# Kernel optimization log

Measured on AMD Instinct MI355X. Metric: run time of the kernel, lower is better.

## Reference

```python
import jax, jax.numpy as jnp
import numpy as np

B, T, D, F, E, K = 2, 1024, 1024, 2048, 8, 2

def setup_inputs() -> dict:
    key = jax.random.key(0)
    ks = jax.random.split(key, 9)
    s = 0.02
    return {
        "states": jax.random.normal(ks[0], (B, T, D), dtype=jnp.float32),
        "Wg": jax.random.normal(ks[1], (D, E), dtype=jnp.float32) * s,
        "W_in": jax.random.normal(ks[2], (E, D, F), dtype=jnp.float32) * s,
        "b_in": jnp.zeros((E, F), dtype=jnp.float32),
        "W_scale": jax.random.normal(ks[3], (E, D, F), dtype=jnp.float32) * s,
        "b_scale": jnp.zeros((E, F), dtype=jnp.float32),
        "W_out": jax.random.normal(ks[4], (E, F, D), dtype=jnp.float32) * s,
        "b_out": jnp.zeros((E, D), dtype=jnp.float32),
        "num_selected": K,
    }

def reference(states, Wg, W_in, b_in, W_scale, b_scale, W_out, b_out, num_selected):
    b, t, d = states.shape
    x = states.reshape(-1, d)                      # [N, D]
    n = x.shape[0]
    # router: softmax over experts, then top-k + renormalize
    probs = jax.nn.softmax(x @ Wg, axis=-1)        # [N, E]
    topw, topi = jax.lax.top_k(probs, num_selected)  # [N, K]
    topw = topw / topw.sum(axis=-1, keepdims=True)
    # dense combine weights [N, E]: zero except selected experts
    w_full = jnp.zeros_like(probs).at[jnp.arange(n)[:, None], topi].set(topw)
    # gated-GELU expert MLPs, batched over experts
    h = jnp.einsum('nd,edf->enf', x, W_in) + b_in[:, None, :]       # [E, N, F]
    s = jnp.einsum('nd,edf->enf', x, W_scale) + b_scale[:, None, :]
    inner = jax.nn.gelu(h, approximate=False) * s                    # exact GELU (torch default)
    y = jnp.einsum('enf,efd->end', inner, W_out) + b_out[:, None, :]  # [E, N, D]
    out = jnp.einsum('end,ne->nd', y, w_full)                         # weighted combine
    return out.reshape(b, t, d)
```

## Files before the change

### kernel.cpp

```cpp
#include <hip/hip_runtime.h>
#include <hip/hip_bf16.h>
#include <math.h>

#define N_TOK 2048
#define DIM   1024
#define FF    2048
#define NEXP  8
#define NSLOT (N_TOK * 2)

typedef __attribute__((ext_vector_type(8))) short short8;
typedef __attribute__((ext_vector_type(4))) float f32x4;

__device__ __forceinline__ unsigned short f2bf(float f) {
    unsigned int u = __float_as_uint(f);
    u += 0x7FFFu + ((u >> 16) & 1u);
    return (unsigned short)(u >> 16);
}

__global__ __launch_bounds__(256) void k_router(const float* __restrict__ x,
        const float* __restrict__ Wg, int* __restrict__ hdr,
        int* __restrict__ tok_e, float* __restrict__ tok_w) {
    int wave = threadIdx.x >> 6, lane = threadIdx.x & 63;
    int t = blockIdx.x * 4 + wave;
    float acc[NEXP];
#pragma unroll
    for (int e = 0; e < NEXP; ++e) acc[e] = 0.f;
    const float* xr = x + (size_t)t * DIM;
    for (int d = lane; d < DIM; d += 64) {
        float xv = xr[d];
        const float* wr = Wg + d * NEXP;
#pragma unroll
        for (int e = 0; e < NEXP; ++e) acc[e] += xv * wr[e];
    }
#pragma unroll
    for (int off = 32; off > 0; off >>= 1) {
#pragma unroll
        for (int e = 0; e < NEXP; ++e) acc[e] += __shfl_down(acc[e], off);
    }
    if (lane == 0) {
        int e0 = 0;
#pragma unroll
        for (int e = 1; e < NEXP; ++e) if (acc[e] > acc[e0]) e0 = e;
        int e1 = -1;
#pragma unroll
        for (int e = 0; e < NEXP; ++e) {
            if (e == e0) continue;
            if (e1 < 0 || acc[e] > acc[e1]) e1 = e;
        }
        float w0 = 1.f / (1.f + expf(acc[e1] - acc[e0]));
        tok_e[2 * t] = e0; tok_e[2 * t + 1] = e1;
        tok_w[2 * t] = w0; tok_w[2 * t + 1] = 1.f - w0;
        atomicAdd(&hdr[e0], 1);
        atomicAdd(&hdr[e1], 1);
    }
}

__global__ void k_scan(int* hdr) {
    if (threadIdx.x == 0 && blockIdx.x == 0) {
        int s = 0;
        for (int e = 0; e < NEXP; ++e) {
            hdr[16 + e] = s;
            hdr[8 + e]  = s;
            s += hdr[e];
        }
        hdr[24] = s;
    }
}

__global__ __launch_bounds__(256) void k_assign(const float* __restrict__ x,
        int* __restrict__ hdr, const int* __restrict__ tok_e,
        const float* __restrict__ tok_w, int* __restrict__ tok_slot,
        float* __restrict__ slot_w, unsigned short* __restrict__ xg) {
    __shared__ int sh[2];
    int t = blockIdx.x;
    if (threadIdx.x == 0) {
        int e0 = tok_e[2 * t], e1 = tok_e[2 * t + 1];
        int p0 = atomicAdd(&hdr[8 + e0], 1);
        int p1 = atomicAdd(&hdr[8 + e1], 1);
        tok_slot[2 * t] = p0; tok_slot[2 * t + 1] = p1;
        slot_w[p0] = tok_w[2 * t];
        slot_w[p1] = tok_w[2 * t + 1];
        sh[0] = p0; sh[1] = p1;
    }
    __syncthreads();
    int s0 = sh[0], s1 = sh[1];
    const float4* xr = (const float4*)(x + (size_t)t * DIM);
    float4 v = xr[threadIdx.x];
    ushort4 b;
    b.x = f2bf(v.x); b.y = f2bf(v.y); b.z = f2bf(v.z); b.w = f2bf(v.w);
    ((ushort4*)(xg + (size_t)s0 * DIM))[threadIdx.x] = b;
    ((ushort4*)(xg + (size_t)s1 * DIM))[threadIdx.x] = b;
}

__global__ __launch_bounds__(256) void k_expert_hs(
        const unsigned short* __restrict__ xg,
        const float* __restrict__ Win, const float* __restrict__ Wsc,
        const float* __restrict__ b_in, const float* __restrict__ b_sc,
        const int* __restrict__ hdr, unsigned short* __restrict__ inner) {
    int e = blockIdx.z;
    int cnt = hdr[e];
    int mtile = blockIdx.y;
    if (mtile * 128 >= cnt) return;
    int base = hdr[16 + e];
    int f0 = blockIdx.x * 64;

    __shared__ unsigned short As[128 * 40];
    __shared__ unsigned short Bh[64 * 40];
    __shared__ unsigned short Bs[64 * 40];

    int tid = threadIdx.x;
    int wave = tid >> 6, lane = tid & 63;
    int lr = lane & 15, lq = lane >> 4;
    int wm = (wave >> 1) * 64, wf = (wave & 1) * 32;

    f32x4 acch[4][2], accs[4][2];
#pragma unroll
    for (int mi = 0; mi < 4; ++mi)
#pragma unroll
        for (int fi = 0; fi < 2; ++fi) {
            acch[mi][fi] = (f32x4){0.f, 0.f, 0.f, 0.f};
            accs[mi][fi] = (f32x4){0.f, 0.f, 0.f, 0.f};
        }

    const unsigned short* Arow = xg + (size_t)(base + mtile * 128) * DIM;
    int ar = tid >> 1, ah = (tid & 1) * 16;
    int bf = tid & 63, bkq = tid >> 6;
    const float* WinE = Win + (size_t)e * DIM * FF;
    const float* WscE = Wsc + (size_t)e * DIM * FF;

    for (int k0 = 0; k0 < DIM; k0 += 32) {
        const uint4* asrc = (const uint4*)(Arow + (size_t)ar * DIM + k0 + ah);
        uint4 a0 = asrc[0], a1 = asrc[1];
        const float* ph = WinE + (size_t)(k0 + bkq * 8) * FF + f0 + bf;
        const float* ps = WscE + (size_t)(k0 + bkq * 8) * FF + f0 + bf;
        unsigned int hv[4], sv[4];
#pragma unroll
        for (int j = 0; j < 4; ++j) {
            hv[j] = (unsigned)f2bf(ph[(size_t)(2 * j) * FF]) |
                    ((unsigned)f2bf(ph[(size_t)(2 * j + 1) * FF]) << 16);
            sv[j] = (unsigned)f2bf(ps[(size_t)(2 * j) * FF]) |
                    ((unsigned)f2bf(ps[(size_t)(2 * j + 1) * FF]) << 16);
        }
        __syncthreads();
        *(uint4*)&As[ar * 40 + ah] = a0;
        *(uint4*)&As[ar * 40 + ah + 8] = a1;
        *(uint4*)&Bh[bf * 40 + bkq * 8] = make_uint4(hv[0], hv[1], hv[2], hv[3]);
        *(uint4*)&Bs[bf * 40 + bkq * 8] = make_uint4(sv[0], sv[1], sv[2], sv[3]);
        __syncthreads();

        short8 af[4], bhf[2], bsf[2];
#pragma unroll
        for (int mi = 0; mi < 4; ++mi)
            af[mi] = *(const short8*)&As[(wm + mi * 16 + lr) * 40 + lq * 8];
#pragma unroll
        for (int fi = 0; fi < 2; ++fi) {
            bhf[fi] = *(const short8*)&Bh[(wf + fi * 16 + lr) * 40 + lq * 8];
            bsf[fi] = *(const short8*)&Bs[(wf + fi * 16 + lr) * 40 + lq * 8];
        }
#pragma unroll
        for (int mi = 0; mi < 4; ++mi)
#pragma unroll
            for (int fi = 0; fi < 2; ++fi) {
                acch[mi][fi] = __builtin_amdgcn_mfma_f32_16x16x32_bf16(
                    af[mi], bhf[fi], acch[mi][fi], 0, 0, 0);
                accs[mi][fi] = __builtin_amdgcn_mfma_f32_16x16x32_bf16(
                    af[mi], bsf[fi], accs[mi][fi], 0, 0, 0);
            }
    }

#pragma unroll
    for (int fi = 0; fi < 2; ++fi) {
        int f = f0 + wf + fi * 16 + lr;
        float bi = b_in[e * FF + f];
        float bs2 = b_sc[e * FF + f];
#pragma unroll
        for (int mi = 0; mi < 4; ++mi) {
#pragma unroll
            for (int r = 0; r < 4; ++r) {
                int rl = wm + mi * 16 + lq * 4 + r;
                int grow = mtile * 128 + rl;
                if (grow < cnt) {
                    float h = acch[mi][fi][r] + bi;
                    float s = accs[mi][fi][r] + bs2;
                    float g = 0.5f * h * (1.f + erff(h * 0.70710678f));
                    inner[(size_t)(base + grow) * FF + f] = f2bf(g * s);
                }
            }
        }
    }
}

__global__ __launch_bounds__(256) void k_expert_out(
        const unsigned short* __restrict__ inner,
        const float* __restrict__ Wout, const float* __restrict__ b_out,
        const int* __restrict__ hdr, const float* __restrict__ slot_w,
        float* __restrict__ ybuf) {
    int e = blockIdx.z;
    int cnt = hdr[e];
    int mtile = blockIdx.y;
    if (mtile * 128 >= cnt) return;
    int base = hdr[16 + e];
    int d0 = blockIdx.x * 128;

    __shared__ unsigned short As[128 * 40];
    __shared__ unsigned short Bt[128 * 40];

    int tid = threadIdx.x;
    int wave = tid >> 6, lane = tid & 63;
    int lr = lane & 15, lq = lane >> 4;
    int wm = (wave >> 1) * 64, wn = (wave & 1) * 64;

    f32x4 acc[4][4];
#pragma unroll
    for (int mi = 0; mi < 4; ++mi)
#pragma unroll
        for (int ni = 0; ni < 4; ++ni) acc[mi][ni] = (f32x4){0.f, 0.f, 0.f, 0.f};

    const unsigned short* Arow = inner + (size_t)(base + mtile * 128) * FF;
    int ar = tid >> 1, ah = (tid & 1) * 16;
    int bd = tid & 127, bkq = tid >> 7;
    const float* W = Wout + (size_t)e * FF * DIM;

    for (int k0 = 0; k0 < FF; k0 += 32) {
        const uint4* asrc = (const uint4*)(Arow + (size_t)ar * FF + k0 + ah);
        uint4 a0 = asrc[0], a1 = asrc[1];
        const float* pw = W + (size_t)(k0 + bkq * 16) * DIM + d0 + bd;
        unsigned int wv[8];
#pragma unroll
        for (int j = 0; j < 8; ++j) {
            wv[j] = (unsigned)f2bf(pw[(size_t)(2 * j) * DIM]) |
                    ((unsigned)f2bf(pw[(size_t)(2 * j + 1) * DIM]) << 16);
        }
        __syncthreads();
        *(uint4*)&As[ar * 40 + ah] = a0;
        *(uint4*)&As[ar * 40 + ah + 8] = a1;
        *(uint4*)&Bt[bd * 40 + bkq * 16] = make_uint4(wv[0], wv[1], wv[2], wv[3]);
        *(uint4*)&Bt[bd * 40 + bkq * 16 + 8] = make_uint4(wv[4], wv[5], wv[6], wv[7]);
        __syncthreads();

        short8 af[4], bfm[4];
#pragma unroll
        for (int mi = 0; mi < 4; ++mi)
            af[mi] = *(const short8*)&As[(wm + mi * 16 + lr) * 40 + lq * 8];
#pragma unroll
        for (int ni = 0; ni < 4; ++ni)
            bfm[ni] = *(const short8*)&Bt[(wn + ni * 16 + lr) * 40 + lq * 8];
#pragma unroll
        for (int mi = 0; mi < 4; ++mi)
#pragma unroll
            for (int ni = 0; ni < 4; ++ni)
                acc[mi][ni] = __builtin_amdgcn_mfma_f32_16x16x32_bf16(
                    af[mi], bfm[ni], acc[mi][ni], 0, 0, 0);
    }

#pragma unroll
    for (int ni = 0; ni < 4; ++ni) {
        int d = d0 + wn + ni * 16 + lr;
        float bo = b_out[e * DIM + d];
#pragma unroll
        for (int mi = 0; mi < 4; ++mi) {
#pragma unroll
            for (int r = 0; r < 4; ++r) {
                int rl = wm + mi * 16 + lq * 4 + r;
                int grow = mtile * 128 + rl;
                if (grow < cnt) {
                    int slot = base + grow;
                    ybuf[(size_t)slot * DIM + d] = (acc[mi][ni][r] + bo) * slot_w[slot];
                }
            }
        }
    }
}

__global__ __launch_bounds__(256) void k_combine(const float* __restrict__ ybuf,
        const int* __restrict__ tok_slot, float* __restrict__ out) {
    int t = blockIdx.x;
    int s0 = tok_slot[2 * t], s1 = tok_slot[2 * t + 1];
    const float4* y0 = (const float4*)(ybuf + (size_t)s0 * DIM);
    const float4* y1 = (const float4*)(ybuf + (size_t)s1 * DIM);
    float4 a = y0[threadIdx.x], b = y1[threadIdx.x];
    float4 r;
    r.x = a.x + b.x; r.y = a.y + b.y; r.z = a.z + b.z; r.w = a.w + b.w;
    ((float4*)(out + (size_t)t * DIM))[threadIdx.x] = r;
}

extern "C" void kernel_launch(void* const* d_in, const int* in_sizes, int n_in,
                              void* d_out, int out_size, void* d_ws, size_t ws_size,
                              hipStream_t stream) {
    (void)in_sizes; (void)n_in; (void)out_size; (void)ws_size;
    const float* x    = (const float*)d_in[0];
    const float* Wg   = (const float*)d_in[1];
    const float* Win  = (const float*)d_in[2];
    const float* b_in = (const float*)d_in[3];
    const float* Wsc  = (const float*)d_in[4];
    const float* b_sc = (const float*)d_in[5];
    const float* Wout = (const float*)d_in[6];
    const float* b_out= (const float*)d_in[7];
    float* out = (float*)d_out;

    char* ws = (char*)d_ws;
    int*   hdr      = (int*)ws;
    int*   tok_e    = (int*)(ws + 256);
    float* tok_w    = (float*)(ws + 16640);
    int*   tok_slot = (int*)(ws + 33024);
    float* slot_w   = (float*)(ws + 49408);
    unsigned short* xg    = (unsigned short*)(ws + 65792);
    unsigned short* inner = (unsigned short*)(ws + 65792 + 8388608);
    float* ybuf = (float*)(ws + 65792 + 8388608 + 16777216);

    hipMemsetAsync(hdr, 0, 256, stream);
    k_router<<<dim3(N_TOK / 4), dim3(256), 0, stream>>>(x, Wg, hdr, tok_e, tok_w);
    k_scan<<<dim3(1), dim3(64), 0, stream>>>(hdr);
    k_assign<<<dim3(N_TOK), dim3(256), 0, stream>>>(x, hdr, tok_e, tok_w, tok_slot, slot_w, xg);
    k_expert_hs<<<dim3(FF / 64, 16, NEXP), dim3(256), 0, stream>>>(xg, Win, Wsc, b_in, b_sc, hdr, inner);
    k_expert_out<<<dim3(DIM / 128, 16, NEXP), dim3(256), 0, stream>>>(inner, Wout, b_out, hdr, slot_w, ybuf);
    k_combine<<<dim3(N_TOK), dim3(256), 0, stream>>>(ybuf, tok_slot, out);
}
```

Before: 498.5 us.

## Prefetch weights, direct-to-LDS A loads, split-K output GEMM with fp16 partials

Both expert GEMMs now load the A tile straight into LDS with global_load_lds and keep a k-major B layout without padding. They also prefetch the next k-step's fp32 weight tile into registers while the MFMAs run. The output GEMM is split in two along K to double the grid, and writes fp16 partial sums. Bias and routing weights are applied in the combine kernel, which removes slot_w. This adds parallelism and overlaps weight latency, at the cost of fp16 rounding of partial sums and extra register pressure under the occupancy-4 launch bounds.

New measurement: 472.0 us. 5.3% less time.

```diff
diff --git a/kernel.cpp b/kernel.cpp
--- a/kernel.cpp
+++ b/kernel.cpp
@@ -10,12 +10,18 @@
 
 typedef __attribute__((ext_vector_type(8))) short short8;
 typedef __attribute__((ext_vector_type(4))) float f32x4;
+typedef _Float16 half_t;
+typedef __attribute__((ext_vector_type(4))) _Float16 h16x4;
 
 __device__ __forceinline__ unsigned short f2bf(float f) {
     unsigned int u = __float_as_uint(f);
     u += 0x7FFFu + ((u >> 16) & 1u);
     return (unsigned short)(u >> 16);
 }
+
+#define GLOAD_LDS16(g, l) \
+    __builtin_amdgcn_global_load_lds((const __attribute__((address_space(1))) unsigned int*)(g), \
+                                     (__attribute__((address_space(3))) unsigned int*)(l), 16, 0, 0)
 
 __global__ __launch_bounds__(256) void k_router(const float* __restrict__ x,
         const float* __restrict__ Wg, int* __restrict__ hdr,
@@ -69,8 +75,7 @@
 
 __global__ __launch_bounds__(256) void k_assign(const float* __restrict__ x,
         int* __restrict__ hdr, const int* __restrict__ tok_e,
-        const float* __restrict__ tok_w, int* __restrict__ tok_slot,
-        float* __restrict__ slot_w, unsigned short* __restrict__ xg) {
+        int* __restrict__ tok_slot, unsigned short* __restrict__ xg) {
     __shared__ int sh[2];
     int t = blockIdx.x;
     if (threadIdx.x == 0) {
@@ -78,8 +83,6 @@
         int p0 = atomicAdd(&hdr[8 + e0], 1);
         int p1 = atomicAdd(&hdr[8 + e1], 1);
         tok_slot[2 * t] = p0; tok_slot[2 * t + 1] = p1;
-        slot_w[p0] = tok_w[2 * t];
-        slot_w[p1] = tok_w[2 * t + 1];
         sh[0] = p0; sh[1] = p1;
     }
     __syncthreads();
@@ -92,7 +95,7 @@
     ((ushort4*)(xg + (size_t)s1 * DIM))[threadIdx.x] = b;
 }
 
-__global__ __launch_bounds__(256) void k_expert_hs(
+__global__ __launch_bounds__(256, 4) void k_expert_hs(
         const unsigned short* __restrict__ xg,
         const float* __restrict__ Win, const float* __restrict__ Wsc,
         const float* __restrict__ b_in, const float* __restrict__ b_sc,
@@ -104,9 +107,9 @@
     int base = hdr[16 + e];
     int f0 = blockIdx.x * 64;
 
-    __shared__ unsigned short As[128 * 40];
-    __shared__ unsigned short Bh[64 * 40];
-    __shared__ unsigned short Bs[64 * 40];
+    __shared__ unsigned short As[128 * 32];
+    __shared__ unsigned short Bh[4 * 64 * 8];
+    __shared__ unsigned short Bs[4 * 64 * 8];
 
     int tid = threadIdx.x;
     int wave = tid >> 6, lane = tid & 63;
@@ -123,17 +126,17 @@
         }
 
     const unsigned short* Arow = xg + (size_t)(base + mtile * 128) * DIM;
-    int ar = tid >> 1, ah = (tid & 1) * 16;
+    int arow = wave * 16 + (lane >> 2);
+    int akk  = (lane & 3) * 8;
+
     int bf = tid & 63, bkq = tid >> 6;
-    const float* WinE = Win + (size_t)e * DIM * FF;
-    const float* WscE = Wsc + (size_t)e * DIM * FF;
-
-    for (int k0 = 0; k0 < DIM; k0 += 32) {
-        const uint4* asrc = (const uint4*)(Arow + (size_t)ar * DIM + k0 + ah);
-        uint4 a0 = asrc[0], a1 = asrc[1];
-        const float* ph = WinE + (size_t)(k0 + bkq * 8) * FF + f0 + bf;
-        const float* ps = WscE + (size_t)(k0 + bkq * 8) * FF + f0 + bf;
-        unsigned int hv[4], sv[4];
+    const float* ph_base = Win + (size_t)e * DIM * FF + f0 + bf;
+    const float* ps_base = Wsc + (size_t)e * DIM * FF + f0 + bf;
+
+    unsigned hv[4], sv[4];
+    {
+        const float* ph = ph_base + (size_t)(bkq * 8) * FF;
+        const float* ps = ps_base + (size_t)(bkq * 8) * FF;
 #pragma unroll
         for (int j = 0; j < 4; ++j) {
             hv[j] = (unsigned)f2bf(ph[(size_t)(2 * j) * FF]) |
@@ -141,21 +144,39 @@
             sv[j] = (unsigned)f2bf(ps[(size_t)(2 * j) * FF]) |
                     ((unsigned)f2bf(ps[(size_t)(2 * j + 1) * FF]) << 16);
         }
+    }
+
+    for (int k0 = 0; k0 < DIM; k0 += 32) {
         __syncthreads();
-        *(uint4*)&As[ar * 40 + ah] = a0;
-        *(uint4*)&As[ar * 40 + ah + 8] = a1;
-        *(uint4*)&Bh[bf * 40 + bkq * 8] = make_uint4(hv[0], hv[1], hv[2], hv[3]);
-        *(uint4*)&Bs[bf * 40 + bkq * 8] = make_uint4(sv[0], sv[1], sv[2], sv[3]);
+        const unsigned short* gA = Arow + (size_t)arow * DIM + k0 + akk;
+        GLOAD_LDS16(gA, &As[(wave * 16) * 32]);
+        GLOAD_LDS16(gA + (size_t)64 * DIM, &As[(64 + wave * 16) * 32]);
+        *(uint4*)&Bh[(bkq * 64 + bf) * 8] = make_uint4(hv[0], hv[1], hv[2], hv[3]);
+        *(uint4*)&Bs[(bkq * 64 + bf) * 8] = make_uint4(sv[0], sv[1], sv[2], sv[3]);
         __syncthreads();
 
+        unsigned hvN[4], svN[4];
+        bool more = (k0 + 32 < DIM);
+        if (more) {
+            const float* ph = ph_base + (size_t)(k0 + 32 + bkq * 8) * FF;
+            const float* ps = ps_base + (size_t)(k0 + 32 + bkq * 8) * FF;
+#pragma unroll
+            for (int j = 0; j < 4; ++j) {
+                hvN[j] = (unsigned)f2bf(ph[(size_t)(2 * j) * FF]) |
+                         ((unsigned)f2bf(ph[(size_t)(2 * j + 1) * FF]) << 16);
+                svN[j] = (unsigned)f2bf(ps[(size_t)(2 * j) * FF]) |
+                         ((unsigned)f2bf(ps[(size_t)(2 * j + 1) * FF]) << 16);
+            }
+        }
+
         short8 af[4], bhf[2], bsf[2];
 #pragma unroll
         for (int mi = 0; mi < 4; ++mi)
-            af[mi] = *(const short8*)&As[(wm + mi * 16 + lr) * 40 + lq * 8];
+            af[mi] = *(const short8*)&As[(wm + mi * 16 + lr) * 32 + lq * 8];
 #pragma unroll
         for (int fi = 0; fi < 2; ++fi) {
-            bhf[fi] = *(const short8*)&Bh[(wf + fi * 16 + lr) * 40 + lq * 8];
-            bsf[fi] = *(const short8*)&Bs[(wf + fi * 16 + lr) * 40 + lq * 8];
+            bhf[fi] = *(const short8*)&Bh[(lq * 64 + wf + fi * 16 + lr) * 8];
+            bsf[fi] = *(const short8*)&Bs[(lq * 64 + wf + fi * 16 + lr) * 8];
         }
 #pragma unroll
         for (int mi = 0; mi < 4; ++mi)
@@ -166,6 +187,10 @@
                 accs[mi][fi] = __builtin_amdgcn_mfma_f32_16x16x32_bf16(
                     af[mi], bsf[fi], accs[mi][fi], 0, 0, 0);
             }
+        if (more) {
+#pragma unroll
+            for (int j = 0; j < 4; ++j) { hv[j] = hvN[j]; sv[j] = svN[j]; }
+        }
     }
 
 #pragma unroll
@@ -190,20 +215,20 @@
     }
 }
 
-__global__ __launch_bounds__(256) void k_expert_out(
+__global__ __launch_bounds__(256, 4) void k_expert_out(
         const unsigned short* __restrict__ inner,
-        const float* __restrict__ Wout, const float* __restrict__ b_out,
-        const int* __restrict__ hdr, const float* __restrict__ slot_w,
-        float* __restrict__ ybuf) {
-    int e = blockIdx.z;
+        const float* __restrict__ Wout,
+        const int* __restrict__ hdr, half_t* __restrict__ pbuf) {
+    int e = blockIdx.z & 7;
+    int ks = blockIdx.z >> 3;
     int cnt = hdr[e];
     int mtile = blockIdx.y;
     if (mtile * 128 >= cnt) return;
     int base = hdr[16 + e];
     int d0 = blockIdx.x * 128;
 
-    __shared__ unsigned short As[128 * 40];
-    __shared__ unsigned short Bt[128 * 40];
+    __shared__ unsigned short As[128 * 32];
+    __shared__ unsigned short Bt[4 * 128 * 8];
 
     int tid = threadIdx.x;
     int wave = tid >> 6, lane = tid & 63;
@@ -217,71 +242,101 @@
         for (int ni = 0; ni < 4; ++ni) acc[mi][ni] = (f32x4){0.f, 0.f, 0.f, 0.f};
 
     const unsigned short* Arow = inner + (size_t)(base + mtile * 128) * FF;
-    int ar = tid >> 1, ah = (tid & 1) * 16;
-    int bd = tid & 127, bkq = tid >> 7;
-    const float* W = Wout + (size_t)e * FF * DIM;
-
-    for (int k0 = 0; k0 < FF; k0 += 32) {
-        const uint4* asrc = (const uint4*)(Arow + (size_t)ar * FF + k0 + ah);
-        uint4 a0 = asrc[0], a1 = asrc[1];
-        const float* pw = W + (size_t)(k0 + bkq * 16) * DIM + d0 + bd;
-        unsigned int wv[8];
-#pragma unroll
-        for (int j = 0; j < 8; ++j) {
+    int arow = wave * 16 + (lane >> 2);
+    int akk  = (lane & 3) * 8;
+
+    int bd = tid & 127, bq = tid >> 7;
+    const float* Wb = Wout + (size_t)e * FF * DIM + d0 + bd;
+
+    int kbeg = ks * (FF / 2), kend = kbeg + FF / 2;
+
+    unsigned wv[8];
+    {
+        const float* pw = Wb + (size_t)(kbeg + bq * 16) * DIM;
+#pragma unroll
+        for (int j = 0; j < 8; ++j)
             wv[j] = (unsigned)f2bf(pw[(size_t)(2 * j) * DIM]) |
                     ((unsigned)f2bf(pw[(size_t)(2 * j + 1) * DIM]) << 16);
-        }
+    }
+
+    for (int k0 = kbeg; k0 < kend; k0 += 32) {
         __syncthreads();
-        *(uint4*)&As[ar * 40 + ah] = a0;
-        *(uint4*)&As[ar * 40 + ah + 8] = a1;
-        *(uint4*)&Bt[bd * 40 + bkq * 16] = make_uint4(wv[0], wv[1], wv[2], wv[3]);
-        *(uint4*)&Bt[bd * 40 + bkq * 16 + 8] = make_uint4(wv[4], wv[5], wv[6], wv[7]);
+        const unsigned short* gA = Arow + (size_t)arow * FF + k0 + akk;
+        GLOAD_LDS16(gA, &As[(wave * 16) * 32]);
+        GLOAD_LDS16(gA + (size_t)64 * FF, &As[(64 + wave * 16) * 32]);
+        *(uint4*)&Bt[((2 * bq) * 128 + bd) * 8]     = make_uint4(wv[0], wv[1], wv[2], wv[3]);
+        *(uint4*)&Bt[((2 * bq + 1) * 128 + bd) * 8] = make_uint4(wv[4], wv[5], wv[6], wv[7]);
         __syncthreads();
 
+        unsigned wvN[8];
+        bool more = (k0 + 32 < kend);
+        if (more) {
+            const float* pw = Wb + (size_t)(k0 + 32 + bq * 16) * DIM;
+#pragma unroll
+            for (int j = 0; j < 8; ++j)
+                wvN[j] = (unsigned)f2bf(pw[(size_t)(2 * j) * DIM]) |
+                         ((unsigned)f2bf(pw[(size_t)(2 * j + 1) * DIM]) << 16);
+        }
+
         short8 af[4], bfm[4];
 #pragma unroll
         for (int mi = 0; mi < 4; ++mi)
-            af[mi] = *(const short8*)&As[(wm + mi * 16 + lr) * 40 + lq * 8];
+            af[mi] = *(const short8*)&As[(wm + mi * 16 + lr) * 32 + lq * 8];
 #pragma unroll
         for (int ni = 0; ni < 4; ++ni)
-            bfm[ni] = *(const short8*)&Bt[(wn + ni * 16 + lr) * 40 + lq * 8];
+            bfm[ni] = *(const short8*)&Bt[(lq * 128 + wn + ni * 16 + lr) * 8];
 #pragma unroll
         for (int mi = 0; mi < 4; ++mi)
 #pragma unroll
             for (int ni = 0; ni < 4; ++ni)
                 acc[mi][ni] = __builtin_amdgcn_mfma_f32_16x16x32_bf16(
                     af[mi], bfm[ni], acc[mi][ni], 0, 0, 0);
-    }
-
+        if (more) {
+#pragma unroll
+            for (int j = 0; j < 8; ++j) wv[j] = wvN[j];
+        }
+    }
+
+    half_t* P = pbuf + (size_t)ks * NSLOT * DIM;
 #pragma unroll
     for (int ni = 0; ni < 4; ++ni) {
         int d = d0 + wn + ni * 16 + lr;
-        float bo = b_out[e * DIM + d];
 #pragma unroll
         for (int mi = 0; mi < 4; ++mi) {
 #pragma unroll
             for (int r = 0; r < 4; ++r) {
                 int rl = wm + mi * 16 + lq * 4 + r;
                 int grow = mtile * 128 + rl;
-                if (grow < cnt) {
-                    int slot = base + grow;
-                    ybuf[(size_t)slot * DIM + d] = (acc[mi][ni][r] + bo) * slot_w[slot];
-                }
+                if (grow < cnt)
+                    P[(size_t)(base + grow) * DIM + d] = (half_t)acc[mi][ni][r];
             }
         }
     }
 }
 
-__global__ __launch_bounds__(256) void k_combine(const float* __restrict__ ybuf,
-        const int* __restrict__ tok_slot, float* __restrict__ out) {
+__global__ __launch_bounds__(256) void k_combine(const half_t* __restrict__ pbuf,
+        const int* __restrict__ tok_slot, const int* __restrict__ tok_e,
+        const float* __restrict__ tok_w, const float* __restrict__ b_out,
+        float* __restrict__ out) {
     int t = blockIdx.x;
+    int d = threadIdx.x * 4;
     int s0 = tok_slot[2 * t], s1 = tok_slot[2 * t + 1];
-    const float4* y0 = (const float4*)(ybuf + (size_t)s0 * DIM);
-    const float4* y1 = (const float4*)(ybuf + (size_t)s1 * DIM);
-    float4 a = y0[threadIdx.x], b = y1[threadIdx.x];
+    int e0 = tok_e[2 * t], e1 = tok_e[2 * t + 1];
+    float w0 = tok_w[2 * t], w1 = tok_w[2 * t + 1];
+    const half_t* pA = pbuf;
+    const half_t* pB = pbuf + (size_t)NSLOT * DIM;
+    h16x4 a0 = *(const h16x4*)&pA[(size_t)s0 * DIM + d];
+    h16x4 a1 = *(const h16x4*)&pB[(size_t)s0 * DIM + d];
+    h16x4 c0 = *(const h16x4*)&pA[(size_t)s1 * DIM + d];
+    h16x4 c1 = *(const h16x4*)&pB[(size_t)s1 * DIM + d];
+    float4 b0 = *(const float4*)&b_out[e0 * DIM + d];
+    float4 b1 = *(const float4*)&b_out[e1 * DIM + d];
     float4 r;
-    r.x = a.x + b.x; r.y = a.y + b.y; r.z = a.z + b.z; r.w = a.w + b.w;
-    ((float4*)(out + (size_t)t * DIM))[threadIdx.x] = r;
+    r.x = w0 * ((float)a0.x + (float)a1.x + b0.x) + w1 * ((float)c0.x + (float)c1.x + b1.x);
+    r.y = w0 * ((float)a0.y + (float)a1.y + b0.y) + w1 * ((float)c0.y + (float)c1.y + b1.y);
+    r.z = w0 * ((float)a0.z + (float)a1.z + b0.z) + w1 * ((float)c0.z + (float)c1.z + b1.z);
+    r.w = w0 * ((float)a0.w + (float)a1.w + b0.w) + w1 * ((float)c0.w + (float)c1.w + b1.w);
+    *(float4*)&out[(size_t)t * DIM + d] = r;
 }
 
 extern "C" void kernel_launch(void* const* d_in, const int* in_sizes, int n_in,
@@ -303,16 +358,15 @@
     int*   tok_e    = (int*)(ws + 256);
     float* tok_w    = (float*)(ws + 16640);
     int*   tok_slot = (int*)(ws + 33024);
-    float* slot_w   = (float*)(ws + 49408);
     unsigned short* xg    = (unsigned short*)(ws + 65792);
     unsigned short* inner = (unsigned short*)(ws + 65792 + 8388608);
-    float* ybuf = (float*)(ws + 65792 + 8388608 + 16777216);
+    half_t* pbuf = (half_t*)(ws + 65792 + 8388608 + 16777216);
 
     hipMemsetAsync(hdr, 0, 256, stream);
     k_router<<<dim3(N_TOK / 4), dim3(256), 0, stream>>>(x, Wg, hdr, tok_e, tok_w);
     k_scan<<<dim3(1), dim3(64), 0, stream>>>(hdr);
-    k_assign<<<dim3(N_TOK), dim3(256), 0, stream>>>(x, hdr, tok_e, tok_w, tok_slot, slot_w, xg);
+    k_assign<<<dim3(N_TOK), dim3(256), 0, stream>>>(x, hdr, tok_e, tok_slot, xg);
     k_expert_hs<<<dim3(FF / 64, 16, NEXP), dim3(256), 0, stream>>>(xg, Win, Wsc, b_in, b_sc, hdr, inner);
-    k_expert_out<<<dim3(DIM / 128, 16, NEXP), dim3(256), 0, stream>>>(inner, Wout, b_out, hdr, slot_w, ybuf);
-    k_combine<<<dim3(N_TOK), dim3(256), 0, stream>>>(ybuf, tok_slot, out);
-}
+    k_expert_out<<<dim3(DIM / 128, 16, NEXP * 2), dim3(256), 0, stream>>>(inner, Wout, hdr, pbuf);
+    k_combine<<<dim3(N_TOK), dim3(256), 0, stream>>>(pbuf, tok_slot, tok_e, tok_w, b_out, out);
+}
```
